# Kernel tuning notes

Hardware: AMD Instinct MI355X
Metric: run time of the kernel (lower is better)

The kernel has to match this reference:

```python
import jax, jax.numpy as jnp
import numpy as np

T, H, I, E = 4096, 1024, 512, 16


def setup_inputs() -> dict:
    key = jax.random.key(0)
    k1, k2, k3 = jax.random.split(key, 3)
    x = jax.random.normal(k1, (T, H), dtype=jnp.float32)
    gate_up_proj = jax.random.normal(k2, (E, H, 2 * I), dtype=jnp.float32) * 0.02
    down_proj = jax.random.normal(k3, (E, I, H), dtype=jnp.float32) * 0.02
    # uneven expert token counts summing exactly to T (no padding rows)
    rng = np.random.default_rng(0)
    raw = rng.integers(64, 512, size=E)
    counts = (raw * T) // raw.sum()
    counts[-1] += T - counts.sum()
    num_tokens_per_expert = jnp.asarray(counts, dtype=jnp.int32)
    return {"x": x, "gate_up_proj": gate_up_proj, "down_proj": down_proj,
            "num_tokens_per_expert": num_tokens_per_expert}


def reference(x, gate_up_proj, down_proj, num_tokens_per_expert):
    # tokens are sorted by expert; build per-token expert id (jit-safe: fixed length)
    n_tok = x.shape[0]
    n_exp = gate_up_proj.shape[0]
    seg = jnp.repeat(jnp.arange(n_exp), num_tokens_per_expert, total_repeat_length=n_tok)  # [T]

    def body(acc, ew):
        e, w_gu, w_d = ew
        xe = jnp.where((seg == e)[:, None], x, jnp.zeros((), x.dtype))  # [T, H], zero rows for other experts
        gu = xe @ w_gu                                                  # [T, 2I]
        g, u = jnp.split(gu, 2, axis=-1)
        o = (jax.nn.silu(g) * u) @ w_d                                  # [T, H]; masked rows stay exactly 0
        return acc + o, None

    init = jnp.zeros((n_tok, down_proj.shape[-1]), x.dtype)
    out, _ = jax.lax.scan(body, init, (jnp.arange(n_exp), gate_up_proj, down_proj))
    return out
```

## Files before the change

### kernel.cpp

```cpp
#include <hip/hip_runtime.h>

#define T_TOK 4096
#define H_DIM 1024
#define I_DIM 512
#define E_EXP 16
#define BM    128
#define BK    64
#define BSTR  68

using bf16x8   = __attribute__((ext_vector_type(8))) short;
using floatx4  = __attribute__((ext_vector_type(4))) float;
using ushort4v = __attribute__((ext_vector_type(4))) unsigned short;

__device__ __forceinline__ unsigned short f2bf(float f) {
  union { float f; unsigned u; } v; v.f = f;
  return (unsigned short)((v.u + 0x7FFFu + ((v.u >> 16) & 1u)) >> 16);
}
__device__ __forceinline__ unsigned pk2(float a, float b) {
  return (unsigned)f2bf(a) | ((unsigned)f2bf(b) << 16);
}

__device__ __forceinline__ void gld16(const void* g, void* l) {
  __builtin_amdgcn_global_load_lds((const __attribute__((address_space(1))) void*)g,
                                   (__attribute__((address_space(3))) void*)l,
                                   16, 0, 0);
}

__device__ __forceinline__ void bar_lgkm() {
  asm volatile("s_waitcnt lgkmcnt(0)" ::: "memory");
  __builtin_amdgcn_sched_barrier(0);
  __builtin_amdgcn_s_barrier();
  __builtin_amdgcn_sched_barrier(0);
}
__device__ __forceinline__ void bar_full() {
  asm volatile("s_waitcnt vmcnt(0) lgkmcnt(0)" ::: "memory");
  __builtin_amdgcn_sched_barrier(0);
  __builtin_amdgcn_s_barrier();
  __builtin_amdgcn_sched_barrier(0);
}

__device__ __forceinline__ bool tile_info(const int* __restrict__ counts, int by,
                                          int& e, int& row0, int& base, int& cnt) {
  int acc = 0, off = 0;
  e = -1;
  #pragma unroll
  for (int i = 0; i < E_EXP; ++i) {
    int c = counts[i];
    int nt = (c + BM - 1) >> 7;
    if (e < 0 && by < acc + nt) { e = i; row0 = (by - acc) * BM; base = off; cnt = c; }
    acc += nt; off += c;
  }
  return e >= 0;
}

__global__ void k_cvt(const float* __restrict__ x, unsigned short* __restrict__ xb) {
  const float4* s4 = (const float4*)x;
  int b0 = blockIdx.x * 512 + threadIdx.x;
  float4 a = s4[b0];
  float4 b = s4[b0 + 256];
  ushort4v oa, ob;
  oa.x = f2bf(a.x); oa.y = f2bf(a.y); oa.z = f2bf(a.z); oa.w = f2bf(a.w);
  ob.x = f2bf(b.x); ob.y = f2bf(b.y); ob.z = f2bf(b.z); ob.w = f2bf(b.w);
  ((ushort4v*)xb)[b0] = oa;
  ((ushort4v*)xb)[b0 + 256] = ob;
}

__launch_bounds__(256, 3)
__global__ void k_gemm_a(const unsigned short* __restrict__ xb,
                         const float* __restrict__ wgu,
                         unsigned short* __restrict__ hb,
                         const int* __restrict__ counts) {
  __shared__ unsigned short As[2][BM * BK];
  __shared__ unsigned short Bs[BM * BSTR];

  int e, row0, base, cnt;
  if (!tile_info(counts, blockIdx.y, e, row0, base, cnt)) return;
  const int rows = (cnt - row0 < BM) ? (cnt - row0) : BM;
  const int c0 = blockIdx.x * 64;

  const int tid = threadIdx.x;
  const int w = tid >> 6, l = tid & 63;
  const int lr = l & 15, q = l >> 4;
  const int asr = l >> 3;
  const int akc = ((l & 7) ^ asr) * 8;
  const int cswz = lr & 7;

  const int nl4 = (tid & 31) * 4;
  const int kb8 = (tid >> 5) * 8;
  const int gc4 = (nl4 < 64) ? (c0 + nl4) : (I_DIM + c0 + nl4 - 64);
  const float* wmat = wgu + (size_t)e * H_DIM * (2 * I_DIM) + gc4;
  unsigned int* BsD = (unsigned int*)Bs;
  const int bd0 = nl4 * (BSTR / 2) + (kb8 >> 1);

  const int mhalf = w & 1, nhalf = w >> 1;
  const int mrow = mhalf * 64;
  const unsigned short* arow = xb + (size_t)(base + row0) * H_DIM;

  int agr[4];
  #pragma unroll
  for (int t = 0; t < 4; ++t) {
    int r = w * 32 + t * 8 + asr;
    agr[t] = (r < rows) ? r : rows - 1;
  }

  floatx4 accg[4][2], accu[4][2];
  #pragma unroll
  for (int i = 0; i < 4; ++i)
    #pragma unroll
    for (int j = 0; j < 2; ++j) { accg[i][j] = (floatx4){0,0,0,0}; accu[i][j] = (floatx4){0,0,0,0}; }

  float4 bv4[8];

  auto loadB = [&](int kk) {
    #pragma unroll
    for (int j = 0; j < 8; ++j)
      bv4[j] = *(const float4*)&wmat[(size_t)(kk + kb8 + j) * (2 * I_DIM)];
  };
  auto loadA = [&](int kk, int buf) {
    #pragma unroll
    for (int t = 0; t < 4; ++t)
      gld16(&arow[(size_t)agr[t] * H_DIM + kk + akc], &As[buf][(w * 32 + t * 8) * BK]);
  };
  auto writeB = [&]() {
    #pragma unroll
    for (int c = 0; c < 4; ++c) {
      uint2 d0, d1;
      d0.x = pk2(bv4[0][c], bv4[1][c]); d0.y = pk2(bv4[2][c], bv4[3][c]);
      d1.x = pk2(bv4[4][c], bv4[5][c]); d1.y = pk2(bv4[6][c], bv4[7][c]);
      *(uint2*)&BsD[bd0 + c * (BSTR / 2)]     = d0;
      *(uint2*)&BsD[bd0 + c * (BSTR / 2) + 2] = d1;
    }
  };
  auto compute = [&](int cb) {
    #pragma unroll
    for (int kf = 0; kf < 2; ++kf) {
      const int c = kf * 4 + q;
      const int ca = (c ^ cswz) * 8;
      const int ch = c * 8;
      bf16x8 af[4], bg[2], bu[2];
      #pragma unroll
      for (int mi = 0; mi < 4; ++mi)
        af[mi] = *(const bf16x8*)&As[cb][(mrow + mi * 16 + lr) * BK + ca];
      #pragma unroll
      for (int ni = 0; ni < 2; ++ni) {
        bg[ni] = *(const bf16x8*)&Bs[(nhalf * 32 + ni * 16 + lr) * BSTR + ch];
        bu[ni] = *(const bf16x8*)&Bs[(64 + nhalf * 32 + ni * 16 + lr) * BSTR + ch];
      }
      #pragma unroll
      for (int mi = 0; mi < 4; ++mi)
        #pragma unroll
        for (int ni = 0; ni < 2; ++ni) {
          accg[mi][ni] = __builtin_amdgcn_mfma_f32_16x16x32_bf16(af[mi], bg[ni], accg[mi][ni], 0, 0, 0);
          accu[mi][ni] = __builtin_amdgcn_mfma_f32_16x16x32_bf16(af[mi], bu[ni], accu[mi][ni], 0, 0, 0);
        }
    }
  };

  loadB(0);
  loadA(0, 0);
  writeB();
  __syncthreads();

  const int nk = H_DIM / BK;
  int cur = 0;
  for (int ki = 0; ki < nk - 1; ++ki) {
    const int kk = (ki + 1) * BK;
    loadB(kk);
    loadA(kk, cur ^ 1);
    __builtin_amdgcn_sched_barrier(0);
    compute(cur);
    bar_lgkm();
    writeB();
    bar_full();
    cur ^= 1;
  }
  compute(cur);

  #pragma unroll
  for (int mi = 0; mi < 4; ++mi)
    #pragma unroll
    for (int r = 0; r < 4; ++r) {
      int row_local = mrow + mi * 16 + q * 4 + r;
      if (row_local >= rows) continue;
      size_t orow = (size_t)(base + row0 + row_local) * I_DIM;
      #pragma unroll
      for (int ni = 0; ni < 2; ++ni) {
        float g = accg[mi][ni][r], u = accu[mi][ni][r];
        float s = g / (1.0f + __expf(-g)) * u;
        hb[orow + c0 + nhalf * 32 + ni * 16 + lr] = f2bf(s);
      }
    }
}

__launch_bounds__(256, 3)
__global__ void k_gemm_b(const unsigned short* __restrict__ hb,
                         const float* __restrict__ wdn,
                         float* __restrict__ out,
                         const int* __restrict__ counts) {
  __shared__ unsigned short As[2][BM * BK];
  __shared__ unsigned short Bs[BM * BSTR];

  int e, row0, base, cnt;
  if (!tile_info(counts, blockIdx.y, e, row0, base, cnt)) return;
  const int rows = (cnt - row0 < BM) ? (cnt - row0) : BM;
  const int n0 = blockIdx.x * 128;

  const int tid = threadIdx.x;
  const int w = tid >> 6, l = tid & 63;
  const int lr = l & 15, q = l >> 4;
  const int asr = l >> 3;
  const int akc = ((l & 7) ^ asr) * 8;
  const int cswz = lr & 7;

  const int nl4 = (tid & 31) * 4;
  const int kb8 = (tid >> 5) * 8;
  const float* wmat = wdn + (size_t)e * I_DIM * H_DIM + n0 + nl4;
  unsigned int* BsD = (unsigned int*)Bs;
  const int bd0 = nl4 * (BSTR / 2) + (kb8 >> 1);

  const int mhalf = w & 1, nhalf = w >> 1;
  const int mrow = mhalf * 64;
  const unsigned short* arow = hb + (size_t)(base + row0) * I_DIM;

  int agr[4];
  #pragma unroll
  for (int t = 0; t < 4; ++t) {
    int r = w * 32 + t * 8 + asr;
    agr[t] = (r < rows) ? r : rows - 1;
  }

  floatx4 acc[4][4];
  #pragma unroll
  for (int i = 0; i < 4; ++i)
    #pragma unroll
    for (int j = 0; j < 4; ++j) acc[i][j] = (floatx4){0,0,0,0};

  float4 bv4[8];

  auto loadB = [&](int kk) {
    #pragma unroll
    for (int j = 0; j < 8; ++j)
      bv4[j] = *(const float4*)&wmat[(size_t)(kk + kb8 + j) * H_DIM];
  };
  auto loadA = [&](int kk, int buf) {
    #pragma unroll
    for (int t = 0; t < 4; ++t)
      gld16(&arow[(size_t)agr[t] * I_DIM + kk + akc], &As[buf][(w * 32 + t * 8) * BK]);
  };
  auto writeB = [&]() {
    #pragma unroll
    for (int c = 0; c < 4; ++c) {
      uint2 d0, d1;
      d0.x = pk2(bv4[0][c], bv4[1][c]); d0.y = pk2(bv4[2][c], bv4[3][c]);
      d1.x = pk2(bv4[4][c], bv4[5][c]); d1.y = pk2(bv4[6][c], bv4[7][c]);
      *(uint2*)&BsD[bd0 + c * (BSTR / 2)]     = d0;
      *(uint2*)&BsD[bd0 + c * (BSTR / 2) + 2] = d1;
    }
  };
  auto compute = [&](int cb) {
    #pragma unroll
    for (int kf = 0; kf < 2; ++kf) {
      const int c = kf * 4 + q;
      const int ca = (c ^ cswz) * 8;
      const int ch = c * 8;
      bf16x8 af[4], bf[4];
      #pragma unroll
      for (int mi = 0; mi < 4; ++mi)
        af[mi] = *(const bf16x8*)&As[cb][(mrow + mi * 16 + lr) * BK + ca];
      #pragma unroll
      for (int ni = 0; ni < 4; ++ni)
        bf[ni] = *(const bf16x8*)&Bs[(nhalf * 64 + ni * 16 + lr) * BSTR + ch];
      #pragma unroll
      for (int mi = 0; mi < 4; ++mi)
        #pragma unroll
        for (int ni = 0; ni < 4; ++ni)
          acc[mi][ni] = __builtin_amdgcn_mfma_f32_16x16x32_bf16(af[mi], bf[ni], acc[mi][ni], 0, 0, 0);
    }
  };

  loadB(0);
  loadA(0, 0);
  writeB();
  __syncthreads();

  const int nk = I_DIM / BK;
  int cur = 0;
  for (int ki = 0; ki < nk - 1; ++ki) {
    const int kk = (ki + 1) * BK;
    loadB(kk);
    loadA(kk, cur ^ 1);
    __builtin_amdgcn_sched_barrier(0);
    compute(cur);
    bar_lgkm();
    writeB();
    bar_full();
    cur ^= 1;
  }
  compute(cur);

  #pragma unroll
  for (int mi = 0; mi < 4; ++mi)
    #pragma unroll
    for (int r = 0; r < 4; ++r) {
      int row_local = mrow + mi * 16 + q * 4 + r;
      if (row_local >= rows) continue;
      size_t orow = (size_t)(base + row0 + row_local) * H_DIM;
      #pragma unroll
      for (int ni = 0; ni < 4; ++ni)
        out[orow + n0 + nhalf * 64 + ni * 16 + lr] = acc[mi][ni][r];
    }
}

extern "C" void kernel_launch(void* const* d_in, const int* in_sizes, int n_in,
                              void* d_out, int out_size, void* d_ws, size_t ws_size,
                              hipStream_t stream) {
  const float* x      = (const float*)d_in[0];
  const float* wgu    = (const float*)d_in[1];
  const float* wdn    = (const float*)d_in[2];
  const int*   counts = (const int*)d_in[3];
  float* out = (float*)d_out;

  unsigned char* ws = (unsigned char*)d_ws;
  unsigned short* xb = (unsigned short*)(ws);
  unsigned short* hb = (unsigned short*)(ws + 8388608);

  k_cvt<<<2048, 256, 0, stream>>>(x, xb);
  k_gemm_a<<<dim3(I_DIM / 64, 48), 256, 0, stream>>>(xb, wgu, hb, counts);
  k_gemm_b<<<dim3(H_DIM / 128, 48), 256, 0, stream>>>(hb, wdn, out, counts);
}
```

Baseline: 178.6 us.

## Double-buffer B weight registers two stages deep and remap blocks for XCD locality

Both GEMM kernels now prefetch the fp32 weight tile two K-steps ahead into alternating register sets. Each step waits with vmcnt(8) instead of draining all outstanding global loads, so weight loads overlap more compute. The 2D grid is flattened to 384 blocks and remapped so blocks landing on the same XCD share an expert's weight columns, which should improve L2 reuse. The extra register set raises VGPR pressure, which may cut occupancy under launch_bounds(256,3), and the vmcnt count depends on the exact load count being correct.

```diff
diff --git a/kernel.cpp b/kernel.cpp
--- a/kernel.cpp
+++ b/kernel.cpp
@@ -1,6 +1,5 @@
 #include <hip/hip_runtime.h>
 
-#define T_TOK 4096
 #define H_DIM 1024
 #define I_DIM 512
 #define E_EXP 16
@@ -32,7 +31,13 @@
   __builtin_amdgcn_s_barrier();
   __builtin_amdgcn_sched_barrier(0);
 }
-__device__ __forceinline__ void bar_full() {
+__device__ __forceinline__ void bar_v8() {
+  asm volatile("s_waitcnt vmcnt(8) lgkmcnt(0)" ::: "memory");
+  __builtin_amdgcn_sched_barrier(0);
+  __builtin_amdgcn_s_barrier();
+  __builtin_amdgcn_sched_barrier(0);
+}
+__device__ __forceinline__ void bar_v0() {
   asm volatile("s_waitcnt vmcnt(0) lgkmcnt(0)" ::: "memory");
   __builtin_amdgcn_sched_barrier(0);
   __builtin_amdgcn_s_barrier();
@@ -51,6 +56,12 @@
     acc += nt; off += c;
   }
   return e >= 0;
+}
+
+__device__ __forceinline__ void xcd2d(int id, int& bx, int& by) {
+  int r = id & 7, j = id >> 3;
+  bx = ((r & 3) << 1) | (j & 1);
+  by = ((r >> 2) * 24) + (j >> 1);
 }
 
 __global__ void k_cvt(const float* __restrict__ x, unsigned short* __restrict__ xb) {
@@ -73,10 +84,12 @@
   __shared__ unsigned short As[2][BM * BK];
   __shared__ unsigned short Bs[BM * BSTR];
 
+  int bx, by;
+  xcd2d(blockIdx.x, bx, by);
   int e, row0, base, cnt;
-  if (!tile_info(counts, blockIdx.y, e, row0, base, cnt)) return;
+  if (!tile_info(counts, by, e, row0, base, cnt)) return;
   const int rows = (cnt - row0 < BM) ? (cnt - row0) : BM;
-  const int c0 = blockIdx.x * 64;
+  const int c0 = bx * 64;
 
   const int tid = threadIdx.x;
   const int w = tid >> 6, l = tid & 63;
@@ -109,24 +122,24 @@
     #pragma unroll
     for (int j = 0; j < 2; ++j) { accg[i][j] = (floatx4){0,0,0,0}; accu[i][j] = (floatx4){0,0,0,0}; }
 
-  float4 bv4[8];
-
-  auto loadB = [&](int kk) {
+  float4 bvA[8], bvB[8];
+
+  auto loadB = [&](int kk, float4 (&bv)[8]) {
     #pragma unroll
     for (int j = 0; j < 8; ++j)
-      bv4[j] = *(const float4*)&wmat[(size_t)(kk + kb8 + j) * (2 * I_DIM)];
+      bv[j] = *(const float4*)&wmat[(size_t)(kk + kb8 + j) * (2 * I_DIM)];
   };
   auto loadA = [&](int kk, int buf) {
     #pragma unroll
     for (int t = 0; t < 4; ++t)
       gld16(&arow[(size_t)agr[t] * H_DIM + kk + akc], &As[buf][(w * 32 + t * 8) * BK]);
   };
-  auto writeB = [&]() {
+  auto writeB = [&](float4 (&bv)[8]) {
     #pragma unroll
     for (int c = 0; c < 4; ++c) {
       uint2 d0, d1;
-      d0.x = pk2(bv4[0][c], bv4[1][c]); d0.y = pk2(bv4[2][c], bv4[3][c]);
-      d1.x = pk2(bv4[4][c], bv4[5][c]); d1.y = pk2(bv4[6][c], bv4[7][c]);
+      d0.x = pk2(bv[0][c], bv[1][c]); d0.y = pk2(bv[2][c], bv[3][c]);
+      d1.x = pk2(bv[4][c], bv[5][c]); d1.y = pk2(bv[6][c], bv[7][c]);
       *(uint2*)&BsD[bd0 + c * (BSTR / 2)]     = d0;
       *(uint2*)&BsD[bd0 + c * (BSTR / 2) + 2] = d1;
     }
@@ -156,24 +169,40 @@
     }
   };
 
-  loadB(0);
+  loadB(0, bvA);
   loadA(0, 0);
-  writeB();
-  __syncthreads();
-
-  const int nk = H_DIM / BK;
+  loadB(BK, bvB);
+  writeB(bvA);
+  bar_v8();
   int cur = 0;
-  for (int ki = 0; ki < nk - 1; ++ki) {
-    const int kk = (ki + 1) * BK;
-    loadB(kk);
-    loadA(kk, cur ^ 1);
+
+  #pragma unroll 1
+  for (int i = 0; i < 7; ++i) {
+    const int t = 2 * i;
+    loadA((t + 1) * BK, cur ^ 1);
+    loadB((t + 2) * BK, bvA);
     __builtin_amdgcn_sched_barrier(0);
     compute(cur);
     bar_lgkm();
-    writeB();
-    bar_full();
+    writeB(bvB);
+    bar_v8();
     cur ^= 1;
-  }
+    loadA((t + 2) * BK, cur ^ 1);
+    loadB((t + 3) * BK, bvB);
+    __builtin_amdgcn_sched_barrier(0);
+    compute(cur);
+    bar_lgkm();
+    writeB(bvA);
+    bar_v8();
+    cur ^= 1;
+  }
+  loadA(15 * BK, cur ^ 1);
+  __builtin_amdgcn_sched_barrier(0);
+  compute(cur);
+  bar_lgkm();
+  writeB(bvB);
+  bar_v0();
+  cur ^= 1;
   compute(cur);
 
   #pragma unroll
@@ -200,10 +229,12 @@
   __shared__ unsigned short As[2][BM * BK];
   __shared__ unsigned short Bs[BM * BSTR];
 
+  int bx, by;
+  xcd2d(blockIdx.x, bx, by);
   int e, row0, base, cnt;
-  if (!tile_info(counts, blockIdx.y, e, row0, base, cnt)) return;
+  if (!tile_info(counts, by, e, row0, base, cnt)) return;
   const int rows = (cnt - row0 < BM) ? (cnt - row0) : BM;
-  const int n0 = blockIdx.x * 128;
+  const int n0 = bx * 128;
 
   const int tid = threadIdx.x;
   const int w = tid >> 6, l = tid & 63;
@@ -235,24 +266,24 @@
     #pragma unroll
     for (int j = 0; j < 4; ++j) acc[i][j] = (floatx4){0,0,0,0};
 
-  float4 bv4[8];
-
-  auto loadB = [&](int kk) {
+  float4 bvA[8], bvB[8];
+
+  auto loadB = [&](int kk, float4 (&bv)[8]) {
     #pragma unroll
     for (int j = 0; j < 8; ++j)
-      bv4[j] = *(const float4*)&wmat[(size_t)(kk + kb8 + j) * H_DIM];
+      bv[j] = *(const float4*)&wmat[(size_t)(kk + kb8 + j) * H_DIM];
   };
   auto loadA = [&](int kk, int buf) {
     #pragma unroll
     for (int t = 0; t < 4; ++t)
       gld16(&arow[(size_t)agr[t] * I_DIM + kk + akc], &As[buf][(w * 32 + t * 8) * BK]);
   };
-  auto writeB = [&]() {
+  auto writeB = [&](float4 (&bv)[8]) {
     #pragma unroll
     for (int c = 0; c < 4; ++c) {
       uint2 d0, d1;
-      d0.x = pk2(bv4[0][c], bv4[1][c]); d0.y = pk2(bv4[2][c], bv4[3][c]);
-      d1.x = pk2(bv4[4][c], bv4[5][c]); d1.y = pk2(bv4[6][c], bv4[7][c]);
+      d0.x = pk2(bv[0][c], bv[1][c]); d0.y = pk2(bv[2][c], bv[3][c]);
+      d1.x = pk2(bv[4][c], bv[5][c]); d1.y = pk2(bv[6][c], bv[7][c]);
       *(uint2*)&BsD[bd0 + c * (BSTR / 2)]     = d0;
       *(uint2*)&BsD[bd0 + c * (BSTR / 2) + 2] = d1;
     }
@@ -278,24 +309,40 @@
     }
   };
 
-  loadB(0);
+  loadB(0, bvA);
   loadA(0, 0);
-  writeB();
-  __syncthreads();
-
-  const int nk = I_DIM / BK;
+  loadB(BK, bvB);
+  writeB(bvA);
+  bar_v8();
   int cur = 0;
-  for (int ki = 0; ki < nk - 1; ++ki) {
-    const int kk = (ki + 1) * BK;
-    loadB(kk);
-    loadA(kk, cur ^ 1);
+
+  #pragma unroll 1
+  for (int i = 0; i < 3; ++i) {
+    const int t = 2 * i;
+    loadA((t + 1) * BK, cur ^ 1);
+    loadB((t + 2) * BK, bvA);
     __builtin_amdgcn_sched_barrier(0);
     compute(cur);
     bar_lgkm();
-    writeB();
-    bar_full();
+    writeB(bvB);
+    bar_v8();
     cur ^= 1;
-  }
+    loadA((t + 2) * BK, cur ^ 1);
+    loadB((t + 3) * BK, bvB);
+    __builtin_amdgcn_sched_barrier(0);
+    compute(cur);
+    bar_lgkm();
+    writeB(bvA);
+    bar_v8();
+    cur ^= 1;
+  }
+  loadA(7 * BK, cur ^ 1);
+  __builtin_amdgcn_sched_barrier(0);
+  compute(cur);
+  bar_lgkm();
+  writeB(bvB);
+  bar_v0();
+  cur ^= 1;
   compute(cur);
 
   #pragma unroll
@@ -325,6 +372,6 @@
   unsigned short* hb = (unsigned short*)(ws + 8388608);
 
   k_cvt<<<2048, 256, 0, stream>>>(x, xb);
-  k_gemm_a<<<dim3(I_DIM / 64, 48), 256, 0, stream>>>(xb, wgu, hb, counts);
-  k_gemm_b<<<dim3(H_DIM / 128, 48), 256, 0, stream>>>(hb, wdn, out, counts);
-}
+  k_gemm_a<<<384, 256, 0, stream>>>(xb, wgu, hb, counts);
+  k_gemm_b<<<384, 256, 0, stream>>>(hb, wdn, out, counts);
+}
```

Measured after the change: 252.7 us. +41.5%, slower.
